# Kernel optimization log

Measured on AMD Instinct MI355X. Metric: run time of the kernel, lower is better.

## Reference

```python
import jax, jax.numpy as jnp
import numpy as np

B, W, C, E, H, V = 128, 128, 32, 20, 64, 256


def setup_inputs() -> dict:
    key = jax.random.key(0)
    ks = jax.random.split(key, 12)
    # sentence lengths (in words) and word lengths (in chars); pads appended
    sent_lens = jax.random.randint(ks[0], (B,), 1, W + 1)
    word_valid = jnp.arange(W)[None, :] < sent_lens[:, None]            # [B,W]
    raw_lens = jax.random.randint(ks[1], (B, W), 1, C + 1)
    lengths = jnp.where(word_valid, raw_lens, 0)                        # [B,W]
    vals = jax.random.randint(ks[2], (B, W, C), 1, V)
    chars = jnp.where(jnp.arange(C)[None, None, :] < lengths[..., None], vals, 0).astype(jnp.int32)
    emb_table = (jax.random.normal(ks[3], (V, E), jnp.float32) * 0.1).at[0].set(0.0)  # padding_idx=0 row is zero
    def xavier(k, shape):
        fan_in, fan_out = shape[1], shape[0]
        lim = np.sqrt(6.0 / (fan_in + fan_out))
        return jax.random.uniform(k, shape, jnp.float32, -lim, lim)
    return dict(
        chars=chars,
        emb_table=emb_table,
        w_ih_f=xavier(ks[4], (4 * H, E)), w_hh_f=xavier(ks[5], (4 * H, H)),
        b_ih_f=jnp.zeros((4 * H,), jnp.float32), b_hh_f=jnp.zeros((4 * H,), jnp.float32),
        w_ih_b=xavier(ks[6], (4 * H, E)), w_hh_b=xavier(ks[7], (4 * H, H)),
        b_ih_b=jnp.zeros((4 * H,), jnp.float32), b_hh_b=jnp.zeros((4 * H,), jnp.float32),
    )


def _char_bilstm_words(chars, emb_table, w_ih_f, w_hh_f, b_ih_f, b_hh_f,
                       w_ih_b, w_hh_b, b_ih_b, b_hh_b):
    Bn, Wn, Cn = chars.shape
    Hn = w_hh_f.shape[1]
    x = emb_table[chars]                              # [B,W,C,E]
    lengths = jnp.sum(chars != 0, axis=-1)            # [B,W]; padding char embeds to 0
    N = Bn * Wn
    xf = x.reshape(N, Cn, -1)                         # flatten all words: [N,C,E]
    lens = lengths.reshape(N)
    bias_f = b_ih_f + b_hh_f

    def step(carry, x_t):
        h, c = carry
        g = x_t @ w_ih_f.T + h @ w_hh_f.T + bias_f    # [N,4H], torch gate order i,f,g,o
        i, f, gg, o = jnp.split(g, 4, axis=-1)
        c = jax.nn.sigmoid(f) * c + jax.nn.sigmoid(i) * jnp.tanh(gg)
        h = jax.nn.sigmoid(o) * jnp.tanh(c)
        return (h, c), h

    h0 = jnp.zeros((N, Hn), x.dtype)
    _, hs = jax.lax.scan(step, (h0, h0), xf.transpose(1, 0, 2))   # [C,N,H]
    idx = jnp.maximum(lens - 1, 0)
    h_fwd = hs[idx, jnp.arange(N)]                                # fwd hidden at last valid char
    # backward direction output at t=len-1: one LSTM step on the last char from zero state
    x_last = jnp.take_along_axis(xf, idx[:, None, None], axis=1)[:, 0, :]   # [N,E]
    gb = x_last @ w_ih_b.T + (b_ih_b + b_hh_b)
    ib, fb, ggb, ob = jnp.split(gb, 4, axis=-1)
    cb = jax.nn.sigmoid(ib) * jnp.tanh(ggb)                       # f gate * 0 initial cell drops out
    h_bwd = jax.nn.sigmoid(ob) * jnp.tanh(cb)
    out = jnp.concatenate([h_fwd, h_bwd], axis=-1)                # [N,2H]
    out = out * (lens > 0)[:, None].astype(out.dtype)             # pad words -> zeros
    return out.reshape(Bn, Wn, 2 * Hn)


def reference(chars, emb_table, w_ih_f, w_hh_f, b_ih_f, b_hh_f,
              w_ih_b, w_hh_b, b_ih_b, b_hh_b):
    return _char_bilstm_words(chars, emb_table, w_ih_f, w_hh_f, b_ih_f, b_hh_f,
                              w_ih_b, w_hh_b, b_ih_b, b_hh_b)
```

## Files before the change

### kernel.cpp

```cpp
#include <hip/hip_runtime.h>
#include <hip/hip_bf16.h>
#include <stdint.h>

#define LOG2E 1.4426950408889634f

__device__ __forceinline__ float fast_sig(float x) {
    float e = __builtin_amdgcn_exp2f(-LOG2E * x);
    return __builtin_amdgcn_rcpf(1.0f + e);
}
__device__ __forceinline__ float fast_tanh(float x) {
    float e = __builtin_amdgcn_exp2f(2.0f * LOG2E * x);
    return 1.0f - 2.0f * __builtin_amdgcn_rcpf(e + 1.0f);
}
__device__ __forceinline__ float rl_f(float v, int k) {
    return __int_as_float(__builtin_amdgcn_readlane(__float_as_int(v), k));
}

__global__ void build_tables(const float* __restrict__ emb,
                             const float* __restrict__ w_ih_f, const float* __restrict__ b_ih_f,
                             const float* __restrict__ b_hh_f,
                             const float* __restrict__ w_ih_b, const float* __restrict__ b_ih_b,
                             const float* __restrict__ b_hh_b,
                             float* __restrict__ xproj, float* __restrict__ hbwd) {
    int v = blockIdx.x;
    int j = threadIdx.x;
    float e[20];
#pragma unroll
    for (int t = 0; t < 20; ++t) e[t] = emb[v * 20 + t];
    float sf[4], sb[4];
#pragma unroll
    for (int g = 0; g < 4; ++g) {
        int row = g * 64 + j;
        float a = b_ih_f[row] + b_hh_f[row];
        float b = b_ih_b[row] + b_hh_b[row];
#pragma unroll
        for (int t = 0; t < 20; ++t) {
            a += e[t] * w_ih_f[row * 20 + t];
            b += e[t] * w_ih_b[row * 20 + t];
        }
        sf[g] = a; sb[g] = b;
    }
    ((float4*)xproj)[v * 64 + j] = make_float4(sf[0], sf[1], sf[2], sf[3]);
    float cb = fast_sig(sb[0]) * fast_tanh(sb[2]);
    hbwd[v * 64 + j] = fast_sig(sb[3]) * fast_tanh(cb);
}

__global__ void count_lens(const int* __restrict__ chars, int* __restrict__ lens,
                           int* __restrict__ cnt) {
    int w = blockIdx.x * blockDim.x + threadIdx.x;
    if (w >= 16384) return;
    int len = 0;
#pragma unroll
    for (int t = 0; t < 32; ++t) len += (chars[w * 32 + t] != 0);
    lens[w] = len;
    if (len > 0) atomicAdd(&cnt[len], 1);
}

__global__ void scan_buckets(const int* __restrict__ cnt, int* __restrict__ cursor,
                             int* __restrict__ nv) {
    if (threadIdx.x == 0) {
        int run = 0;
        for (int L = 1; L <= 32; ++L) { cursor[L] = run; run += cnt[L]; }
        *nv = run;
    }
}

__global__ void scatter_ids(const int* __restrict__ lens, int* __restrict__ cursor,
                            int* __restrict__ sorted) {
    int w = blockIdx.x * blockDim.x + threadIdx.x;
    if (w >= 16384) return;
    int len = lens[w];
    if (len > 0) {
        int pos = atomicAdd(&cursor[len], 1);
        sorted[pos] = w;
    }
}

__launch_bounds__(256, 2)
__global__ void bilstm_main(const int* __restrict__ chars, const float* __restrict__ w_hh,
                            const float4* __restrict__ xproj, const float* __restrict__ hbwd,
                            const int* __restrict__ sorted, const int* __restrict__ nvp,
                            float* __restrict__ out) {
    __shared__ float lds[16384];
    const int nv = *nvp;
    if (blockIdx.x * 32 >= nv) return;
    const int tid = threadIdx.x;
    for (int i = tid; i < 16384; i += 256) {
        int row = i >> 6, k = i & 63;
        lds[(((k << 6) | (row & 63)) << 2) | (row >> 6)] = w_hh[i];
    }
    __syncthreads();

    const int wave = tid >> 6, lane = tid & 63;
    const int base = (blockIdx.x * 4 + wave) * 8;
    const int nw = min(8, nv - base);
    if (nw <= 0) return;

    int idv = 0;
    if (lane < 8 && base + lane < nv) idv = sorted[base + lane];

    int wid[8], ch[8], len[8];
#pragma unroll
    for (int g = 0; g < 8; ++g) {
        wid[g] = __builtin_amdgcn_readlane(idv, g);
        int c = 0;
        if (lane < 32) c = chars[wid[g] * 32 + lane];
        ch[g] = c;
        unsigned long long m = __ballot(c != 0);
        len[g] = (g < nw) ? __popcll(m) : 0;
    }
    int maxlen = 0;
#pragma unroll
    for (int g = 0; g < 8; ++g) maxlen = max(maxlen, len[g]);

    float h[8], cc[8];
#pragma unroll
    for (int g = 0; g < 8; ++g) { h[g] = 0.0f; cc[g] = 0.0f; }

    const float4* ldsw = (const float4*)lds;

    for (int t = 0; t < maxlen; ++t) {
        float4 xp[8];
#pragma unroll
        for (int g = 0; g < 8; ++g) {
            int ct = __builtin_amdgcn_readlane(ch[g], t);
            xp[g] = xproj[ct * 64 + lane];
        }
        float4 acc[8];
#pragma unroll
        for (int g = 0; g < 8; ++g) acc[g] = make_float4(0.f, 0.f, 0.f, 0.f);
#pragma unroll 4
        for (int k = 0; k < 64; ++k) {
            float4 w4 = ldsw[(k << 6) + lane];
#pragma unroll
            for (int g = 0; g < 8; ++g) {
                float hk = rl_f(h[g], k);
                acc[g].x += hk * w4.x;
                acc[g].y += hk * w4.y;
                acc[g].z += hk * w4.z;
                acc[g].w += hk * w4.w;
            }
        }
#pragma unroll
        for (int g = 0; g < 8; ++g) {
            float gi = fast_sig(acc[g].x + xp[g].x);
            float gf = fast_sig(acc[g].y + xp[g].y);
            float gg = fast_tanh(acc[g].z + xp[g].z);
            float go = fast_sig(acc[g].w + xp[g].w);
            float cn = gf * cc[g] + gi * gg;
            float hn = go * fast_tanh(cn);
            bool act = (t < len[g]);
            cc[g] = act ? cn : cc[g];
            h[g] = act ? hn : h[g];
        }
    }

#pragma unroll
    for (int g = 0; g < 8; ++g) {
        if (g < nw) {
            int cl = __builtin_amdgcn_readlane(ch[g], len[g] - 1);
            float hb = hbwd[cl * 64 + lane];
            out[wid[g] * 128 + lane] = h[g];
            out[wid[g] * 128 + 64 + lane] = hb;
        }
    }
}

extern "C" void kernel_launch(void* const* d_in, const int* in_sizes, int n_in,
                              void* d_out, int out_size, void* d_ws, size_t ws_size,
                              hipStream_t stream) {
    const int* chars    = (const int*)d_in[0];
    const float* emb    = (const float*)d_in[1];
    const float* w_ih_f = (const float*)d_in[2];
    const float* w_hh_f = (const float*)d_in[3];
    const float* b_ih_f = (const float*)d_in[4];
    const float* b_hh_f = (const float*)d_in[5];
    const float* w_ih_b = (const float*)d_in[6];
    const float* b_ih_b = (const float*)d_in[8];
    const float* b_hh_b = (const float*)d_in[9];
    float* out = (float*)d_out;

    float* wsf   = (float*)d_ws;
    float* xproj = wsf;
    float* hbwd  = wsf + 65536;
    int* iws     = (int*)(wsf + 65536 + 16384);
    int* lens    = iws;
    int* sorted  = iws + 16384;
    int* cnt     = iws + 32768;
    int* cursor  = iws + 32801;
    int* nv      = iws + 32834;

    hipMemsetAsync(d_out, 0, (size_t)out_size * sizeof(float), stream);
    hipMemsetAsync(cnt, 0, 33 * sizeof(int), stream);
    build_tables<<<256, 64, 0, stream>>>(emb, w_ih_f, b_ih_f, b_hh_f,
                                         w_ih_b, b_ih_b, b_hh_b, xproj, hbwd);
    count_lens<<<64, 256, 0, stream>>>(chars, lens, cnt);
    scan_buckets<<<1, 64, 0, stream>>>(cnt, cursor, nv);
    scatter_ids<<<64, 256, 0, stream>>>(lens, cursor, sorted);
    bilstm_main<<<512, 256, 0, stream>>>(chars, w_hh_f, (const float4*)xproj,
                                         hbwd, sorted, nv, out);
}
```

Baseline: 227.6 us.

## Halve words per wave, pretranspose W_hh once, and ballot-based length counting

The main LSTM kernel now handles 4 words per wave instead of 8 and launches twice as many blocks, so more waves work concurrently and each wave has a shorter critical path. The recurrent weight matrix is transposed into the gate-interleaved layout once inside build_tables, so each block only does a coalesced float4 copy into LDS instead of a scattered transpose. count_lens now uses one lane per character with a ballot and popcount instead of a serial 32-load loop per thread. The trade-off is that every block reloads the full 64KB weight tile into LDS, and there are now twice as many such loads in total.

```diff
diff --git a/kernel.cpp b/kernel.cpp
--- a/kernel.cpp
+++ b/kernel.cpp
@@ -21,9 +21,15 @@
                              const float* __restrict__ b_hh_f,
                              const float* __restrict__ w_ih_b, const float* __restrict__ b_ih_b,
                              const float* __restrict__ b_hh_b,
-                             float* __restrict__ xproj, float* __restrict__ hbwd) {
+                             const float* __restrict__ w_hh_f,
+                             float* __restrict__ xproj, float* __restrict__ hbwd,
+                             float* __restrict__ wt) {
     int v = blockIdx.x;
     int j = threadIdx.x;
+    int d = v * 64 + j;
+    int tk = d >> 8, tj = (d >> 2) & 63, tg = d & 3;
+    wt[d] = w_hh_f[(((tg << 6) | tj) << 6) | tk];
+
     float e[20];
 #pragma unroll
     for (int t = 0; t < 20; ++t) e[t] = emb[v * 20 + t];
@@ -47,13 +53,16 @@
 
 __global__ void count_lens(const int* __restrict__ chars, int* __restrict__ lens,
                            int* __restrict__ cnt) {
-    int w = blockIdx.x * blockDim.x + threadIdx.x;
-    if (w >= 16384) return;
-    int len = 0;
-#pragma unroll
-    for (int t = 0; t < 32; ++t) len += (chars[w * 32 + t] != 0);
-    lens[w] = len;
-    if (len > 0) atomicAdd(&cnt[len], 1);
+    int word = blockIdx.x * 8 + (threadIdx.x >> 5);
+    int c = threadIdx.x & 31;
+    int v = chars[word * 32 + c];
+    unsigned long long m = __ballot(v != 0);
+    int hi = (threadIdx.x >> 5) & 1;
+    int len = __popcll(m & (hi ? 0xFFFFFFFF00000000ULL : 0x00000000FFFFFFFFULL));
+    if (c == 0) {
+        lens[word] = len;
+        if (len > 0) atomicAdd(&cnt[len], 1);
+    }
 }
 
 __global__ void scan_buckets(const int* __restrict__ cnt, int* __restrict__ cursor,
@@ -77,31 +86,28 @@
 }
 
 __launch_bounds__(256, 2)
-__global__ void bilstm_main(const int* __restrict__ chars, const float* __restrict__ w_hh,
+__global__ void bilstm_main(const int* __restrict__ chars, const float4* __restrict__ wt,
                             const float4* __restrict__ xproj, const float* __restrict__ hbwd,
                             const int* __restrict__ sorted, const int* __restrict__ nvp,
                             float* __restrict__ out) {
-    __shared__ float lds[16384];
+    __shared__ float4 ldsw[4096];
     const int nv = *nvp;
-    if (blockIdx.x * 32 >= nv) return;
+    if (blockIdx.x * 16 >= nv) return;
     const int tid = threadIdx.x;
-    for (int i = tid; i < 16384; i += 256) {
-        int row = i >> 6, k = i & 63;
-        lds[(((k << 6) | (row & 63)) << 2) | (row >> 6)] = w_hh[i];
-    }
+    for (int i = tid; i < 4096; i += 256) ldsw[i] = wt[i];
     __syncthreads();
 
     const int wave = tid >> 6, lane = tid & 63;
-    const int base = (blockIdx.x * 4 + wave) * 8;
-    const int nw = min(8, nv - base);
+    const int base = (blockIdx.x * 4 + wave) * 4;
+    const int nw = min(4, nv - base);
     if (nw <= 0) return;
 
     int idv = 0;
-    if (lane < 8 && base + lane < nv) idv = sorted[base + lane];
-
-    int wid[8], ch[8], len[8];
-#pragma unroll
-    for (int g = 0; g < 8; ++g) {
+    if (lane < 4 && base + lane < nv) idv = sorted[base + lane];
+
+    int wid[4], ch[4], len[4];
+#pragma unroll
+    for (int g = 0; g < 4; ++g) {
         wid[g] = __builtin_amdgcn_readlane(idv, g);
         int c = 0;
         if (lane < 32) c = chars[wid[g] * 32 + lane];
@@ -111,38 +117,36 @@
     }
     int maxlen = 0;
 #pragma unroll
-    for (int g = 0; g < 8; ++g) maxlen = max(maxlen, len[g]);
-
-    float h[8], cc[8];
-#pragma unroll
-    for (int g = 0; g < 8; ++g) { h[g] = 0.0f; cc[g] = 0.0f; }
-
-    const float4* ldsw = (const float4*)lds;
+    for (int g = 0; g < 4; ++g) maxlen = max(maxlen, len[g]);
+
+    float h[4], cc[4];
+#pragma unroll
+    for (int g = 0; g < 4; ++g) { h[g] = 0.0f; cc[g] = 0.0f; }
 
     for (int t = 0; t < maxlen; ++t) {
-        float4 xp[8];
-#pragma unroll
-        for (int g = 0; g < 8; ++g) {
+        float4 xp[4];
+#pragma unroll
+        for (int g = 0; g < 4; ++g) {
             int ct = __builtin_amdgcn_readlane(ch[g], t);
             xp[g] = xproj[ct * 64 + lane];
         }
-        float4 acc[8];
-#pragma unroll
-        for (int g = 0; g < 8; ++g) acc[g] = make_float4(0.f, 0.f, 0.f, 0.f);
-#pragma unroll 4
+        float4 acc[4];
+#pragma unroll
+        for (int g = 0; g < 4; ++g) acc[g] = make_float4(0.f, 0.f, 0.f, 0.f);
+#pragma unroll 8
         for (int k = 0; k < 64; ++k) {
             float4 w4 = ldsw[(k << 6) + lane];
 #pragma unroll
-            for (int g = 0; g < 8; ++g) {
+            for (int g = 0; g < 4; ++g) {
                 float hk = rl_f(h[g], k);
-                acc[g].x += hk * w4.x;
-                acc[g].y += hk * w4.y;
-                acc[g].z += hk * w4.z;
-                acc[g].w += hk * w4.w;
+                acc[g].x = fmaf(hk, w4.x, acc[g].x);
+                acc[g].y = fmaf(hk, w4.y, acc[g].y);
+                acc[g].z = fmaf(hk, w4.z, acc[g].z);
+                acc[g].w = fmaf(hk, w4.w, acc[g].w);
             }
         }
 #pragma unroll
-        for (int g = 0; g < 8; ++g) {
+        for (int g = 0; g < 4; ++g) {
             float gi = fast_sig(acc[g].x + xp[g].x);
             float gf = fast_sig(acc[g].y + xp[g].y);
             float gg = fast_tanh(acc[g].z + xp[g].z);
@@ -156,7 +160,7 @@
     }
 
 #pragma unroll
-    for (int g = 0; g < 8; ++g) {
+    for (int g = 0; g < 4; ++g) {
         if (g < nw) {
             int cl = __builtin_amdgcn_readlane(ch[g], len[g] - 1);
             float hb = hbwd[cl * 64 + lane];
@@ -183,20 +187,23 @@
     float* wsf   = (float*)d_ws;
     float* xproj = wsf;
     float* hbwd  = wsf + 65536;
-    int* iws     = (int*)(wsf + 65536 + 16384);
+    float* wt    = wsf + 65536 + 16384;
+    int* iws     = (int*)(wt + 16384);
     int* lens    = iws;
     int* sorted  = iws + 16384;
     int* cnt     = iws + 32768;
     int* cursor  = iws + 32801;
     int* nv      = iws + 32834;
 
-    hipMemsetAsync(d_out, 0, (size_t)out_size * sizeof(float), stream);
-    hipMemsetAsync(cnt, 0, 33 * sizeof(int), stream);
+    (void)hipMemsetAsync(d_out, 0, (size_t)out_size * sizeof(float), stream);
+    (void)hipMemsetAsync(cnt, 0, 33 * sizeof(int), stream);
     build_tables<<<256, 64, 0, stream>>>(emb, w_ih_f, b_ih_f, b_hh_f,
-                                         w_ih_b, b_ih_b, b_hh_b, xproj, hbwd);
-    count_lens<<<64, 256, 0, stream>>>(chars, lens, cnt);
+                                         w_ih_b, b_ih_b, b_hh_b, w_hh_f,
+                                         xproj, hbwd, wt);
+    count_lens<<<2048, 256, 0, stream>>>(chars, lens, cnt);
     scan_buckets<<<1, 64, 0, stream>>>(cnt, cursor, nv);
     scatter_ids<<<64, 256, 0, stream>>>(lens, cursor, sorted);
-    bilstm_main<<<512, 256, 0, stream>>>(chars, w_hh_f, (const float4*)xproj,
-                                         hbwd, sorted, nv, out);
-}
+    bilstm_main<<<1024, 256, 0, stream>>>(chars, (const float4*)wt,
+                                          (const float4*)xproj,
+                                          hbwd, sorted, nv, out);
+}
```

Result: faster. 195.4 us (-14.1%).
